# Optimization experiments

Hardware: AMD Instinct MI355X
Metric: run time of the kernel (lower is better)

## Reference

```python
import jax, jax.numpy as jnp
import numpy as np

B, N, E = 4, 4096, 1024
F_IN, F_OUT, F_EDGE = 128, 128, 64


def setup_inputs() -> dict:
    key = jax.random.key(0)
    k1, k2, k3, k4, k5, k6 = jax.random.split(key, 6)
    node = jax.random.normal(k1, (B, N, F_IN), dtype=jnp.float32)
    edge = jax.random.normal(k2, (B, E, F_EDGE), dtype=jnp.float32)
    # symmetric 0/1 adjacency (sparse-ish, avg degree ~ 2*0.005*N)
    a = (jax.random.uniform(k3, (B, N, N)) < 0.005).astype(jnp.float32)
    node_adj = jnp.maximum(a, jnp.swapaxes(a, 1, 2))
    # D: positive diagonal degree matrix [B,N,N]
    deg = node_adj.sum(-1) + 1.0                      # [B,N], strictly > 0
    D = deg[:, :, None] * jnp.eye(N, dtype=jnp.float32)
    # T: node-edge incidence-like 0/1 matrix [B,N,E]
    T = (jax.random.uniform(k4, (B, N, E)) < 0.002).astype(jnp.float32)
    stdv_n = 1.0 / np.sqrt(F_OUT)
    node_weight = jax.random.uniform(k5, (F_IN, F_OUT), minval=-stdv_n, maxval=stdv_n, dtype=jnp.float32)
    stdv_e = 1.0 / np.sqrt(F_EDGE)
    edge_weight = jax.random.uniform(k6, (F_EDGE,), minval=-stdv_e, maxval=stdv_e, dtype=jnp.float32)
    return {"node": node, "edge": edge, "node_adj": node_adj, "D": D, "T": T,
            "edge_weight": edge_weight, "node_weight": node_weight}


def reference(node, edge, node_adj, D, T, edge_weight, node_weight):
    # D <- sqrt(D); nonzero entries inverted (i.e. D^{-1/2}, zeros stay zero)
    nz = D != 0
    Dinv = jnp.where(nz, 1.0 / jnp.sqrt(jnp.where(nz, D, 1.0)), 0.0)
    # node_adj += I  (first bmm(D, node_adj) in the source is dead code)
    A = node_adj + jnp.eye(node_adj.shape[2], dtype=node_adj.dtype)
    A_tilde = jnp.matmul(A, Dinv)                      # [B,N,N]
    # HePe = edge @ edge_weight -> per-edge scalar; T diag(HePe) T^T fused:
    HePe = jnp.einsum('bef,f->be', edge, edge_weight)  # [B,E]
    S = jnp.einsum('bne,be,bme->bnm', T, HePe, T)      # (T*v) @ T^T, [B,N,N]
    out = jnp.matmul(S * A_tilde, node)                # [B,N,F_IN]
    out = jnp.matmul(out, node_weight)                 # [B,N,F_OUT]
    return out
```

## Files before the change

kernel.cpp:

```cpp
#include <hip/hip_runtime.h>

#define BB 4
#define NN 4096
#define EE 1024
#define FIN 128
#define FE 64
#define CAP 33
#define LSTRIDE 34
#define CAPE 40

#define PRE_GEMM 512
#define PRE_HEPE (BB * EE / 4)
#define PRE_DINV (BB * NN / 256)

typedef unsigned short u16;
typedef unsigned int u32;
typedef unsigned long long u64;

__global__ __launch_bounds__(256) void k_pre(const float* __restrict__ edge,
                                             const float* __restrict__ ew,
                                             const float* __restrict__ D,
                                             const float* __restrict__ node,
                                             const float* __restrict__ W,
                                             float* __restrict__ hepe,
                                             int* __restrict__ ecnt,
                                             float* __restrict__ dinv,
                                             float* __restrict__ nodeW,
                                             int withGemm) {
    __shared__ float tile[32][FIN];
    int t = threadIdx.x, lane = t & 63, wid = t >> 6;
    int bid = blockIdx.x;
    if (bid < PRE_HEPE) {
        int row = bid * 4 + wid;
        float v = edge[(size_t)row * FE + lane] * ew[lane];
#pragma unroll
        for (int d = 32; d >= 1; d >>= 1) v += __shfl_xor(v, d, 64);
        if (lane == 0) { hepe[row] = v; ecnt[row] = 0; }
    } else if (bid < PRE_HEPE + PRE_DINV) {
        int idx = (bid - PRE_HEPE) * 256 + t;
        int b = idx >> 12, n = idx & (NN - 1);
        float v = D[((size_t)b * NN + n) * NN + n];
        dinv[idx] = (v != 0.f) ? (1.f / sqrtf(v)) : 0.f;
    } else if (withGemm) {
        size_t row0 = (size_t)(bid - PRE_HEPE - PRE_DINV) * 32;
        const float* sbase = node + row0 * FIN;
        float* dbase = nodeW + row0 * FIN;
#pragma unroll
        for (int k = 0; k < 16; k++) {
            int idx = k * 256 + t;
            tile[idx >> 7][idx & 127] = sbase[idx];
        }
        __syncthreads();
        int f = t & 127, h = t >> 7;
        float acc[16];
#pragma unroll
        for (int j = 0; j < 16; j++) acc[j] = 0.f;
        for (int k = 0; k < 128; k += 2) {
            float w0 = W[k * 128 + f];
            float w1 = W[(k + 1) * 128 + f];
#pragma unroll
            for (int j = 0; j < 16; j++) {
                float2 tv = *(const float2*)&tile[h * 16 + j][k];
                acc[j] += tv.x * w0 + tv.y * w1;
            }
        }
#pragma unroll
        for (int j = 0; j < 16; j++) dbase[(size_t)(h * 16 + j) * 128 + f] = acc[j];
    }
}

__global__ __launch_bounds__(256) void k_lists(const float* __restrict__ T,
                                               u16* __restrict__ lists,
                                               int* __restrict__ ecnt,
                                               u16* __restrict__ elists) {
    int t = threadIdx.x, lane = t & 63, wid = t >> 6;
    int row = blockIdx.x * 4 + wid;
    int b = row >> 12, n = row & (NN - 1);
    const float4* rowT = (const float4*)(T + (size_t)row * EE);
    float4 t0 = rowT[lane], t1 = rowT[64 + lane], t2 = rowT[128 + lane], t3 = rowT[192 + lane];
    float vs[16] = {t0.x, t0.y, t0.z, t0.w, t1.x, t1.y, t1.z, t1.w,
                    t2.x, t2.y, t2.z, t2.w, t3.x, t3.y, t3.z, t3.w};
    int c = 0;
#pragma unroll
    for (int k = 0; k < 16; k++) c += (vs[k] != 0.f);
    int x = c;
#pragma unroll
    for (int d = 1; d < 64; d <<= 1) {
        int o = __shfl_up(x, d, 64);
        if (lane >= d) x += o;
    }
    int tot = __shfl(x, 63, 64);
    int pos = x - c;
    u16* L = lists + (size_t)row * LSTRIDE;
    if (c > 0) {
#pragma unroll
        for (int k = 0; k < 16; k++) {
            if (vs[k] != 0.f) {
                if (pos < CAP) {
                    int e = ((k >> 2) * 64 + lane) * 4 + (k & 3);
                    L[1 + pos] = (u16)e;
                    int eb = (b << 10) + e;
                    int p2 = atomicAdd(&ecnt[eb], 1);
                    if (p2 < CAPE) elists[(size_t)eb * CAPE + p2] = (u16)n;
                }
                pos++;
            }
        }
    }
    if (lane == 0) L[0] = (u16)(tot < CAP ? tot : CAP);
}

__global__ __launch_bounds__(256) void k_gemm(const float* __restrict__ src,
                                              const float* __restrict__ W,
                                              float* __restrict__ dst) {
    __shared__ float tile[32][FIN];
    int t = threadIdx.x;
    size_t row0 = (size_t)blockIdx.x * 32;
    const float* sbase = src + row0 * FIN;
    float* dbase = dst + row0 * FIN;
#pragma unroll
    for (int k = 0; k < 16; k++) {
        int idx = k * 256 + t;
        tile[idx >> 7][idx & 127] = sbase[idx];
    }
    __syncthreads();
    int f = t & 127, h = t >> 7;
    float acc[16];
#pragma unroll
    for (int j = 0; j < 16; j++) acc[j] = 0.f;
    for (int k = 0; k < 128; k += 2) {
        float w0 = W[k * 128 + f];
        float w1 = W[(k + 1) * 128 + f];
#pragma unroll
        for (int j = 0; j < 16; j++) {
            float2 tv = *(const float2*)&tile[h * 16 + j][k];
            acc[j] += tv.x * w0 + tv.y * w1;
        }
    }
#pragma unroll
    for (int j = 0; j < 16; j++) dbase[(size_t)(h * 16 + j) * 128 + f] = acc[j];
}

__global__ __launch_bounds__(256) void k_main(const float* __restrict__ A,
                                              const float* __restrict__ rows,
                                              const float* __restrict__ hepe,
                                              const float* __restrict__ dinv,
                                              const u16* __restrict__ lists,
                                              const int* __restrict__ ecnt,
                                              const u16* __restrict__ elists,
                                              float* __restrict__ out) {
    __shared__ u16   sOFF[4][34];
    __shared__ float sH[4][34];
    __shared__ u32   sEB[4][34];
    int t = threadIdx.x, lane = t & 63, wid = t >> 6;
    int row = blockIdx.x * 4 + wid;
    int b = row >> 12, n = row & (NN - 1);
    const u16* L = lists + (size_t)row * LSTRIDE;

    int cn = L[0];
    int eRaw = 0;
    if (lane <= 32) eRaw = L[1 + lane];
    int eb = (b << 10) + (eRaw & (EE - 1));
    int cnt = 0; float h = 0.f;
    if (lane <= 32) { cnt = ecnt[eb]; h = hepe[eb]; }
    if (lane >= cn) { cnt = 0; h = 0.f; }
    if (cnt > CAPE) cnt = CAPE;

    float sd = h;
#pragma unroll
    for (int d = 32; d >= 1; d >>= 1) sd += __shfl_xor(sd, d, 64);

    int x = cnt;
#pragma unroll
    for (int d = 1; d < 64; d <<= 1) {
        int o = __shfl_up(x, d, 64);
        if (lane >= d) x += o;
    }
    int P = __shfl(x, 63, 64);
    if (lane < cn) {
        sOFF[wid][lane] = (u16)(x - cnt);
        sH[wid][lane]   = h;
        sEB[wid][lane]  = (u32)eb * CAPE;
    }

    float dn    = dinv[row];
    float adiag = A[((size_t)b << 24) + ((size_t)n << 12) + n];
    float cdiag = sd * (adiag + 1.f) * dn;

    const float2* rows2 = (const float2*)rows;
    float2 nvd = rows2[(size_t)row * 64 + lane];
    float2 acc = make_float2(cdiag * nvd.x, cdiag * nvd.y);

    for (int base = 0; base < P; base += 64) {
        int p = base + lane;
        float cc = 0.f; int m = 0;
        if (p < P) {
            int jj = 0;
            while (jj + 1 < cn && sOFF[wid][jj + 1] <= p) jj++;
            m = elists[sEB[wid][jj] + (u32)(p - sOFF[wid][jj])];
            if (m != n) {
                float a = A[((size_t)b << 24) + ((size_t)n << 12) + m];
                if (a != 0.f) cc = sH[wid][jj] * a * dinv[(b << 12) + m];
            }
        }
        u64 mask = __ballot(cc != 0.f);
        while (mask) {
            int src = __ffsll(mask) - 1;
            mask &= mask - 1;
            float cb = __shfl(cc, src, 64);
            int   mb = __shfl(m, src, 64);
            float2 nv = rows2[((size_t)((b << 12) + mb)) * 64 + lane];
            acc.x += cb * nv.x;
            acc.y += cb * nv.y;
        }
    }
    float2* out2 = (float2*)out;
    out2[(size_t)row * 64 + lane] = acc;
}

extern "C" void kernel_launch(void* const* d_in, const int* in_sizes, int n_in,
                              void* d_out, int out_size, void* d_ws, size_t ws_size,
                              hipStream_t stream) {
    const float* node     = (const float*)d_in[0];
    const float* edge     = (const float*)d_in[1];
    const float* node_adj = (const float*)d_in[2];
    const float* D        = (const float*)d_in[3];
    const float* T        = (const float*)d_in[4];
    const float* ew       = (const float*)d_in[5];
    const float* W        = (const float*)d_in[6];
    float* out = (float*)d_out;

    char* ws = (char*)d_ws;
    float* hepe  = (float*)ws;                          ws += BB * EE * 4;
    float* dinv  = (float*)ws;                          ws += BB * NN * 4;
    int*   ecnt  = (int*)ws;                            ws += BB * EE * 4;
    u16*   lists = (u16*)ws;                            ws += BB * NN * LSTRIDE * 2;
    u16*   elists= (u16*)ws;                            ws += BB * EE * CAPE * 2;
    size_t small_need = (size_t)(ws - (char*)d_ws);
    float* nodeW = (float*)ws;
    bool fuse = ws_size >= small_need + (size_t)BB * NN * FIN * 4;

    int preGrid = PRE_HEPE + PRE_DINV + (fuse ? PRE_GEMM : 0);
    k_pre  <<<preGrid,     256, 0, stream>>>(edge, ew, D, node, W,
                                             hepe, ecnt, dinv, nodeW, fuse ? 1 : 0);
    k_lists<<<BB * NN / 4, 256, 0, stream>>>(T, lists, ecnt, elists);

    if (fuse) {
        k_main<<<BB * NN / 4, 256, 0, stream>>>(node_adj, nodeW, hepe, dinv,
                                                lists, ecnt, elists, out);
    } else {
        k_main<<<BB * NN / 4, 256, 0, stream>>>(node_adj, node, hepe, dinv,
                                                lists, ecnt, elists, out);
        k_gemm<<<BB * NN / 32, 256, 0, stream>>>(out, W, out);
    }
}
```

Before: 56.49 us.

## Move node GEMM into list-building kernel and hoist independent loads in main

Splits the pre-pass so hepe, ecnt reset and dinv run in a small kernel. The node×W GEMM blocks now share a launch with the T-row list building, so GEMM compute overlaps the memory-bound T scan instead of sitting on the critical path of the first kernel. In k_main, the dinv, diagonal-A and node-row loads are issued before the list/scan work so their latency is hidden. Kernel count and ordering dependencies stay the same; only the load balance between kernels shifts.

Result: faster. 46.74 us (-17.3%).

```diff
diff --git a/kernel.cpp b/kernel.cpp
--- a/kernel.cpp
+++ b/kernel.cpp
@@ -9,40 +9,46 @@
 #define LSTRIDE 34
 #define CAPE 40
 
-#define PRE_GEMM 512
-#define PRE_HEPE (BB * EE / 4)
-#define PRE_DINV (BB * NN / 256)
-
 typedef unsigned short u16;
 typedef unsigned int u32;
 typedef unsigned long long u64;
 
-__global__ __launch_bounds__(256) void k_pre(const float* __restrict__ edge,
-                                             const float* __restrict__ ew,
-                                             const float* __restrict__ D,
-                                             const float* __restrict__ node,
-                                             const float* __restrict__ W,
-                                             float* __restrict__ hepe,
-                                             int* __restrict__ ecnt,
-                                             float* __restrict__ dinv,
-                                             float* __restrict__ nodeW,
-                                             int withGemm) {
+__global__ __launch_bounds__(256) void k_misc(const float* __restrict__ edge,
+                                              const float* __restrict__ ew,
+                                              const float* __restrict__ D,
+                                              float* __restrict__ hepe,
+                                              int* __restrict__ ecnt,
+                                              float* __restrict__ dinv) {
+    int t = threadIdx.x, lane = t & 63, wid = t >> 6;
+    int bid = blockIdx.x;
+    if (bid < BB * EE / 4) {
+        int row = bid * 4 + wid;
+        float v = edge[(size_t)row * FE + lane] * ew[lane];
+#pragma unroll
+        for (int d = 32; d >= 1; d >>= 1) v += __shfl_xor(v, d, 64);
+        if (lane == 0) { hepe[row] = v; ecnt[row] = 0; }
+    } else {
+        int idx = (bid - BB * EE / 4) * 256 + t;
+        int b = idx >> 12, n = idx & (NN - 1);
+        float v = D[((size_t)b * NN + n) * NN + n];
+        dinv[idx] = (v != 0.f) ? (1.f / sqrtf(v)) : 0.f;
+    }
+}
+
+__global__ __launch_bounds__(256) void k_stage(const float* __restrict__ T,
+                                               const float* __restrict__ node,
+                                               const float* __restrict__ W,
+                                               u16* __restrict__ lists,
+                                               int* __restrict__ ecnt,
+                                               u16* __restrict__ elists,
+                                               float* __restrict__ nodeW,
+                                               int gemmBlocks) {
     __shared__ float tile[32][FIN];
     int t = threadIdx.x, lane = t & 63, wid = t >> 6;
     int bid = blockIdx.x;
-    if (bid < PRE_HEPE) {
-        int row = bid * 4 + wid;
-        float v = edge[(size_t)row * FE + lane] * ew[lane];
-#pragma unroll
-        for (int d = 32; d >= 1; d >>= 1) v += __shfl_xor(v, d, 64);
-        if (lane == 0) { hepe[row] = v; ecnt[row] = 0; }
-    } else if (bid < PRE_HEPE + PRE_DINV) {
-        int idx = (bid - PRE_HEPE) * 256 + t;
-        int b = idx >> 12, n = idx & (NN - 1);
-        float v = D[((size_t)b * NN + n) * NN + n];
-        dinv[idx] = (v != 0.f) ? (1.f / sqrtf(v)) : 0.f;
-    } else if (withGemm) {
-        size_t row0 = (size_t)(bid - PRE_HEPE - PRE_DINV) * 32;
+
+    if (bid < gemmBlocks) {
+        size_t row0 = (size_t)bid * 32;
         const float* sbase = node + row0 * FIN;
         float* dbase = nodeW + row0 * FIN;
 #pragma unroll
@@ -66,48 +72,42 @@
         }
 #pragma unroll
         for (int j = 0; j < 16; j++) dbase[(size_t)(h * 16 + j) * 128 + f] = acc[j];
-    }
-}
-
-__global__ __launch_bounds__(256) void k_lists(const float* __restrict__ T,
-                                               u16* __restrict__ lists,
-                                               int* __restrict__ ecnt,
-                                               u16* __restrict__ elists) {
-    int t = threadIdx.x, lane = t & 63, wid = t >> 6;
-    int row = blockIdx.x * 4 + wid;
-    int b = row >> 12, n = row & (NN - 1);
-    const float4* rowT = (const float4*)(T + (size_t)row * EE);
-    float4 t0 = rowT[lane], t1 = rowT[64 + lane], t2 = rowT[128 + lane], t3 = rowT[192 + lane];
-    float vs[16] = {t0.x, t0.y, t0.z, t0.w, t1.x, t1.y, t1.z, t1.w,
-                    t2.x, t2.y, t2.z, t2.w, t3.x, t3.y, t3.z, t3.w};
-    int c = 0;
-#pragma unroll
-    for (int k = 0; k < 16; k++) c += (vs[k] != 0.f);
-    int x = c;
-#pragma unroll
-    for (int d = 1; d < 64; d <<= 1) {
-        int o = __shfl_up(x, d, 64);
-        if (lane >= d) x += o;
-    }
-    int tot = __shfl(x, 63, 64);
-    int pos = x - c;
-    u16* L = lists + (size_t)row * LSTRIDE;
-    if (c > 0) {
-#pragma unroll
-        for (int k = 0; k < 16; k++) {
-            if (vs[k] != 0.f) {
-                if (pos < CAP) {
-                    int e = ((k >> 2) * 64 + lane) * 4 + (k & 3);
-                    L[1 + pos] = (u16)e;
-                    int eb = (b << 10) + e;
-                    int p2 = atomicAdd(&ecnt[eb], 1);
-                    if (p2 < CAPE) elists[(size_t)eb * CAPE + p2] = (u16)n;
+    } else {
+        int row = (bid - gemmBlocks) * 4 + wid;
+        int b = row >> 12, n = row & (NN - 1);
+        const float4* rowT = (const float4*)(T + (size_t)row * EE);
+        float4 t0 = rowT[lane], t1 = rowT[64 + lane], t2 = rowT[128 + lane], t3 = rowT[192 + lane];
+        float vs[16] = {t0.x, t0.y, t0.z, t0.w, t1.x, t1.y, t1.z, t1.w,
+                        t2.x, t2.y, t2.z, t2.w, t3.x, t3.y, t3.z, t3.w};
+        int c = 0;
+#pragma unroll
+        for (int k = 0; k < 16; k++) c += (vs[k] != 0.f);
+        int x = c;
+#pragma unroll
+        for (int d = 1; d < 64; d <<= 1) {
+            int o = __shfl_up(x, d, 64);
+            if (lane >= d) x += o;
+        }
+        int tot = __shfl(x, 63, 64);
+        int pos = x - c;
+        u16* L = lists + (size_t)row * LSTRIDE;
+        if (c > 0) {
+#pragma unroll
+            for (int k = 0; k < 16; k++) {
+                if (vs[k] != 0.f) {
+                    if (pos < CAP) {
+                        int e = ((k >> 2) * 64 + lane) * 4 + (k & 3);
+                        L[1 + pos] = (u16)e;
+                        int eb = (b << 10) + e;
+                        int p2 = atomicAdd(&ecnt[eb], 1);
+                        if (p2 < CAPE) elists[(size_t)eb * CAPE + p2] = (u16)n;
+                    }
+                    pos++;
                 }
-                pos++;
             }
         }
-    }
-    if (lane == 0) L[0] = (u16)(tot < CAP ? tot : CAP);
+        if (lane == 0) L[0] = (u16)(tot < CAP ? tot : CAP);
+    }
 }
 
 __global__ __launch_bounds__(256) void k_gemm(const float* __restrict__ src,
@@ -157,6 +157,11 @@
     int b = row >> 12, n = row & (NN - 1);
     const u16* L = lists + (size_t)row * LSTRIDE;
 
+    const float2* rows2 = (const float2*)rows;
+    float  dn    = dinv[row];
+    float  adiag = A[((size_t)b << 24) + ((size_t)n << 12) + n];
+    float2 nvd   = rows2[(size_t)row * 64 + lane];
+
     int cn = L[0];
     int eRaw = 0;
     if (lane <= 32) eRaw = L[1 + lane];
@@ -183,12 +188,7 @@
         sEB[wid][lane]  = (u32)eb * CAPE;
     }
 
-    float dn    = dinv[row];
-    float adiag = A[((size_t)b << 24) + ((size_t)n << 12) + n];
     float cdiag = sd * (adiag + 1.f) * dn;
-
-    const float2* rows2 = (const float2*)rows;
-    float2 nvd = rows2[(size_t)row * 64 + lane];
     float2 acc = make_float2(cdiag * nvd.x, cdiag * nvd.y);
 
     for (int base = 0; base < P; base += 64) {
@@ -240,10 +240,11 @@
     float* nodeW = (float*)ws;
     bool fuse = ws_size >= small_need + (size_t)BB * NN * FIN * 4;
 
-    int preGrid = PRE_HEPE + PRE_DINV + (fuse ? PRE_GEMM : 0);
-    k_pre  <<<preGrid,     256, 0, stream>>>(edge, ew, D, node, W,
-                                             hepe, ecnt, dinv, nodeW, fuse ? 1 : 0);
-    k_lists<<<BB * NN / 4, 256, 0, stream>>>(T, lists, ecnt, elists);
+    int gemmBlocks = fuse ? (BB * NN / 32) : 0;
+
+    k_misc <<<BB * EE / 4 + BB * NN / 256,  256, 0, stream>>>(edge, ew, D, hepe, ecnt, dinv);
+    k_stage<<<gemmBlocks + BB * NN / 4,     256, 0, stream>>>(T, node, W, lists, ecnt,
+                                                              elists, nodeW, gemmBlocks);
 
     if (fuse) {
         k_main<<<BB * NN / 4, 256, 0, stream>>>(node_adj, nodeW, hepe, dinv,
```
